# Performance work log

Hardware: AMD Instinct MI355X
Metric: run time of the kernel (lower is better)

The kernel has to match this reference:

```python
import jax, jax.numpy as jnp
import numpy as np

N, D, F, M, K = 4096, 1024, 4096, 2048, 307
EPS = 1e-5

def _ln(h, g, b):
    mu = jnp.mean(h, axis=-1, keepdims=True)
    var = jnp.mean(jnp.square(h - mu), axis=-1, keepdims=True)
    return (h - mu) * jax.lax.rsqrt(var + EPS) * g + b

def _attn(h, wq, wk, wv, mask):
    # wq/wk/wv stored as [D, D] so y = h @ w matches torch Linear(h) with W.T
    q = h @ wq
    k = h @ wk
    v = h @ wv
    s = (q @ k.T) * (1.0 / np.sqrt(D))  # [N, N]
    s = jnp.where(mask, -1e9, s)
    a = jax.nn.softmax(s, axis=-1)
    return a @ v, a

def _ffn(h, w1, b1, w2, b2):
    return jax.nn.gelu(h @ w1 + b1, approximate=False) @ w2 + b2

def setup_inputs() -> dict:
    ks = jax.random.split(jax.random.key(0), 32)
    s = 0.02
    p = lambda i, shape: (jax.random.normal(ks[i], shape, jnp.float32) * s)
    inp = {
        'x': jax.random.normal(ks[0], (N, D), jnp.float32),
        'real_edge_mask': jax.random.bernoulli(ks[1], 0.5, (N, N)),
        'fake_edge_mask': jax.random.bernoulli(ks[2], 0.5, (N, N)),
        'mask_nodes': jax.random.permutation(ks[3], N)[:M].astype(jnp.int32),
        'gene_idx': jnp.argsort(jax.random.uniform(ks[4], (M, D)), axis=-1)[:, :K].astype(jnp.int32),
        'wq1': p(5, (D, D)), 'wk1': p(6, (D, D)), 'wv1': p(7, (D, D)),
        'g1': jnp.ones((D,)), 'be1': jnp.zeros((D,)),
        'fw1': p(8, (D, F)), 'fb1': jnp.zeros((F,)),
        'fw2': p(9, (F, D)), 'fb2': jnp.zeros((D,)),
        'g2': jnp.ones((D,)), 'be2': jnp.zeros((D,)),
        'wq2': p(10, (D, D)), 'wk2': p(11, (D, D)), 'wv2': p(12, (D, D)),
        'g3': jnp.ones((D,)), 'be3': jnp.zeros((D,)),
        'hw1': p(13, (D, F)), 'hb1': jnp.zeros((F,)),
        'hw2': p(14, (F, D)), 'hb2': jnp.zeros((D,)),
        'g4': jnp.ones((D,)), 'be4': jnp.zeros((D,)),
        'head_w': p(15, (D, D)), 'head_b': jnp.zeros((D,)),
    }
    return inp

def reference(x, real_edge_mask, fake_edge_mask, mask_nodes, gene_idx,
              wq1, wk1, wv1, g1, be1, fw1, fb1, fw2, fb2, g2, be2,
              wq2, wk2, wv2, g3, be3, hw1, hb1, hw2, hb2, g4, be4,
              head_w, head_b):
    rows = jnp.arange(M)[:, None]  # [M, 1]
    # encoding_mask_nodes: zero K genes in each of M masked cells
    mask_x = x[mask_nodes].at[rows, gene_idx].set(0.0)
    use_x = x.at[mask_nodes].set(mask_x)

    hidden, encode_weights = _attn(use_x, wq1, wk1, wv1, real_edge_mask)
    hidden = _ln(hidden + use_x, g1, be1)
    hidden = _ln(hidden + _ffn(hidden, fw1, fb1, fw2, fb2), g2, be2)
    # NOTE: original `hidden[mask_nodes][gene_mask] = 0` is a no-op (copy), reproduced.

    recon, _decode_weights = _attn(hidden, wq2, wk2, wv2, real_edge_mask)
    recon = _ln(recon + hidden, g3, be3)
    recon = _ln(recon + _ffn(recon, hw1, hb1, hw2, hb2), g4, be4)
    h = recon @ head_w + head_b

    x_init = x[mask_nodes][rows, gene_idx]   # [M, K]
    x_recon = h[mask_nodes][rows, gene_idx]  # [M, K]
    return x_init, x_recon, encode_weights, recon
```

## Files before the change

kernel.cpp:

```cpp
#include <hip/hip_runtime.h>
#include <math.h>
#include <stdint.h>

typedef unsigned short u16;
typedef __attribute__((ext_vector_type(8))) short bf16x8;
typedef __attribute__((ext_vector_type(4))) float f32x4;
typedef __attribute__((ext_vector_type(4))) unsigned short u16x4;

#define N_ 4096
#define D_ 1024
#define F_ 4096
#define M_ 2048
#define KG 307

__device__ __forceinline__ u16 f2bf(float f) {
  unsigned int u = __float_as_uint(f);
  unsigned int r = u + 0x7fffu + ((u >> 16) & 1u);
  return (u16)(r >> 16);
}

__device__ __forceinline__ float bf2f(u16 u) {
  return __uint_as_float((unsigned)u << 16);
}

__device__ __forceinline__ void gl_lds16(const u16* g, u16* l) {
  __builtin_amdgcn_global_load_lds(
      (__attribute__((address_space(1))) void*)(void*)g,
      (__attribute__((address_space(3))) void*)(void*)l,
      16, 0, 0);
}

enum { E_QKV = 0, E_SMASK = 1, E_PART = 2, E_GELU = 3 };
#define SMEM_BYTES 131072

template <int EPI>
__global__ __launch_bounds__(512, 2) void gemm256(
    const u16* __restrict__ A, const u16* __restrict__ B,
    void* __restrict__ C, void* __restrict__ C2,
    int gridM, int gridN, int Ndim, int Ksp, int lda, int ldb, long zstr,
    const float* __restrict__ bias, const unsigned char* __restrict__ mask,
    float scale) {
  extern __shared__ __align__(16) char smem[];
  const int tid = threadIdx.x;
  const int lane = tid & 63;
  const int wid = tid >> 6;
  const int wr = wid >> 2;
  const int wc = wid & 3;
  const int lr = lane & 15;
  const int lk = lane >> 4;

  const int nwg = gridM * gridN;
  const int bid = blockIdx.x;
  const int q8 = nwg >> 3, r8 = nwg & 7;
  const int xcd = bid & 7, ii = bid >> 3;
  int wg = (xcd < r8 ? xcd * (q8 + 1) : r8 * (q8 + 1) + (xcd - r8) * q8) + ii;
  const int rowblk = wg / (gridN << 2);
  const int rem = wg - rowblk * (gridN << 2);
  const int mrem = gridM - (rowblk << 2);
  int mtile, ntile;
  if (mrem >= 4) {
    ntile = rem >> 2;
    mtile = (rowblk << 2) + (rem & 3);
  } else {
    ntile = rem / mrem;
    mtile = (rowblk << 2) + (rem - ntile * mrem);
  }
  const long bm = (long)mtile * 256;
  const long bn = (long)ntile * 256;
  const long koff = (long)blockIdx.y * Ksp;
  const int NT = Ksp >> 6;

  auto stA = [&](int t, int h) {
    char* base = smem + ((t & 1) << 15) + (h << 14);
    const long k0 = koff + ((long)t << 6);
#pragma unroll
    for (int j = 0; j < 2; ++j) {
      int o = tid + (j << 9);
      int r = o >> 3, s = o & 7;
      gl_lds16(A + (bm + (h << 7) + r) * (long)lda + k0 + ((s ^ (r & 7)) << 3),
               (u16*)(base + o * 16));
    }
  };
  auto stB = [&](int t, int h) {
    char* base = smem + 65536 + ((t & 1) << 15) + (h << 14);
    const long k0 = koff + ((long)t << 6);
#pragma unroll
    for (int j = 0; j < 2; ++j) {
      int o = tid + (j << 9);
      int r = o >> 3, s = o & 7;
      gl_lds16(B + (bn + (h << 7) + r) * (long)ldb + k0 + ((s ^ (r & 7)) << 3),
               (u16*)(base + o * 16));
    }
  };

  bf16x8 avA[2][2], avB[2][2], bv[4][2];
  f32x4 acc[8][4];
#pragma unroll
  for (int m = 0; m < 8; ++m)
#pragma unroll
    for (int n = 0; n < 4; ++n) acc[m][n] = f32x4{0.f, 0.f, 0.f, 0.f};

  auto rdAV = [&](bf16x8(&av)[2][2], const char* Ab_, int q) {
#pragma unroll
    for (int e = 0; e < 2; ++e)
#pragma unroll
      for (int ks = 0; ks < 2; ++ks) {
        int r = (wr << 7) + (q << 5) + (e << 4) + lr;
        av[e][ks] = *(const bf16x8*)(Ab_ + r * 128 + ((((ks << 2) | lk) ^ (r & 7)) << 4));
      }
  };
  auto rdBV = [&](const char* Bb_) {
#pragma unroll
    for (int n = 0; n < 4; ++n)
#pragma unroll
      for (int ks = 0; ks < 2; ++ks) {
        int r = (wc << 6) + (n << 4) + lr;
        bv[n][ks] = *(const bf16x8*)(Bb_ + r * 128 + ((((ks << 2) | lk) ^ (r & 7)) << 4));
      }
  };

#define MM(Q, AV)                                                              \
  __builtin_amdgcn_s_setprio(1);                                               \
  _Pragma("unroll") for (int e = 0; e < 2; ++e)                                \
  _Pragma("unroll") for (int n = 0; n < 4; ++n)                                \
  _Pragma("unroll") for (int ks = 0; ks < 2; ++ks)                             \
      acc[((Q) << 1) | e][n] = __builtin_amdgcn_mfma_f32_16x16x32_bf16(        \
          AV[e][ks], bv[n][ks], acc[((Q) << 1) | e][n], 0, 0, 0);              \
  __builtin_amdgcn_s_setprio(0);                                               \
  __builtin_amdgcn_sched_barrier(0);

  stA(0, 0);
  stA(0, 1);
  stB(0, 0);
  stB(0, 1);
  if (NT > 1) {
    stB(1, 0);
    stB(1, 1);
  }
  __builtin_amdgcn_sched_barrier(0);
  if (NT > 1)
    asm volatile("s_waitcnt vmcnt(4)");
  else
    asm volatile("s_waitcnt vmcnt(0)");
  __builtin_amdgcn_sched_barrier(0);
  __builtin_amdgcn_s_barrier();
  rdAV(avA, smem, 0);
  __builtin_amdgcn_sched_barrier(0);

  for (int t = 0; t < NT; ++t) {
    const char* Ab = smem + ((t & 1) << 15);
    const char* AbN = smem + (((t + 1) & 1) << 15);
    const char* Bb = smem + 65536 + ((t & 1) << 15);
    rdBV(Bb);
    rdAV(avB, Ab, 1);
    if (t + 1 < NT) stA(t + 1, 0);
    __builtin_amdgcn_sched_barrier(0);
    asm volatile("s_waitcnt lgkmcnt(4)");
    __builtin_amdgcn_sched_barrier(0);
    MM(0, avA)
    rdAV(avA, Ab, 2);
    if (t + 1 < NT) stA(t + 1, 1);
    __builtin_amdgcn_sched_barrier(0);
    asm volatile("s_waitcnt lgkmcnt(4)");
    __builtin_amdgcn_sched_barrier(0);
    MM(1, avB)
    __builtin_amdgcn_s_barrier();
    rdAV(avB, Ab, 3);
    if (t + 2 < NT) stB(t + 2, 0);
    __builtin_amdgcn_sched_barrier(0);
    asm volatile("s_waitcnt lgkmcnt(4)");
    __builtin_amdgcn_sched_barrier(0);
    MM(2, avA)
    asm volatile("s_waitcnt lgkmcnt(0)");
    if (t + 2 < NT)
      asm volatile("s_waitcnt vmcnt(2)");
    else
      asm volatile("s_waitcnt vmcnt(0)");
    __builtin_amdgcn_sched_barrier(0);
    __builtin_amdgcn_s_barrier();
    if (t + 1 < NT) rdAV(avA, AbN, 0);
    if (t + 2 < NT) stB(t + 2, 1);
    __builtin_amdgcn_sched_barrier(0);
    MM(3, avB)
  }
#undef MM

  const bool z0 = (blockIdx.y == 0);
#pragma unroll
  for (int m = 0; m < 8; ++m) {
#pragma unroll
    for (int n = 0; n < 4; ++n) {
#pragma unroll
      for (int j = 0; j < 4; ++j) {
        long row = bm + (wr << 7) + (m << 4) + (lk << 2) + j;
        long col = bn + (wc << 6) + (n << 4) + lr;
        float v = acc[m][n][j];
        if constexpr (EPI == E_QKV) {
          if (col < 2048)
            ((u16*)C)[row * 2048 + col] = f2bf(v);
          else
            ((u16*)C2)[(col - 2048) * (long)N_ + row] = f2bf(v);
        } else if constexpr (EPI == E_SMASK) {
          v *= scale;
          if (mask[row * Ndim + col]) v = -1e9f;
          ((u16*)C)[row * Ndim + col] = f2bf(v);
        } else if constexpr (EPI == E_PART) {
          ((u16*)C)[(long)blockIdx.y * zstr + row * Ndim + col] =
              f2bf(v + ((z0 && bias) ? bias[col] : 0.f));
        } else if constexpr (EPI == E_GELU) {
          float tv = v + bias[col];
          float gl = 0.5f * tv * (1.0f + erff(tv * 0.70710678118654752f));
          ((u16*)C)[row * Ndim + col] = f2bf(gl);
        }
      }
    }
  }
}

__global__ __launch_bounds__(256) void gemm_nt_bias(
    const u16* __restrict__ A, const u16* __restrict__ B, float* __restrict__ C,
    int Ndim, int K, int lda, int ldb, const float* __restrict__ bias) {
  __shared__ u16 As[2][128 * 32];
  __shared__ u16 Bs[2][128 * 32];
  const int tid = threadIdx.x;
  const int lane = tid & 63;
  const int wid = tid >> 6;
  const int wr = wid >> 1;
  const int wc = wid & 1;
  const int lr = lane & 15;
  const int lk = lane >> 4;
  const long bm = (long)blockIdx.x * 128;
  const long bn = (long)blockIdx.y * 128;

  f32x4 acc[4][4];
#pragma unroll
  for (int i = 0; i < 4; ++i)
#pragma unroll
    for (int j = 0; j < 4; ++j) acc[i][j] = f32x4{0.f, 0.f, 0.f, 0.f};

  auto stage = [&](int buf, long k0) {
#pragma unroll
    for (int i = 0; i < 2; ++i) {
      int c = tid + i * 256;
      gl_lds16(A + (bm + (c >> 2)) * (long)lda + k0 + (c & 3) * 8, As[buf] + c * 8);
    }
#pragma unroll
    for (int i = 0; i < 2; ++i) {
      int c = tid + i * 256;
      gl_lds16(B + (bn + (c >> 2)) * (long)ldb + k0 + (c & 3) * 8, Bs[buf] + c * 8);
    }
  };

  stage(0, 0);
  __syncthreads();
  const int nt = K / 32;
  int cur = 0;
  for (int t = 0; t < nt; ++t) {
    if (t + 1 < nt) stage(cur ^ 1, (long)(t + 1) * 32);
    bf16x8 av[4], bv[4];
#pragma unroll
    for (int mr = 0; mr < 4; ++mr)
      av[mr] = *(const bf16x8*)(As[cur] + (wr * 64 + mr * 16 + lr) * 32 + lk * 8);
#pragma unroll
    for (int nr = 0; nr < 4; ++nr)
      bv[nr] = *(const bf16x8*)(Bs[cur] + (wc * 64 + nr * 16 + lr) * 32 + lk * 8);
#pragma unroll
    for (int mr = 0; mr < 4; ++mr)
#pragma unroll
      for (int nr = 0; nr < 4; ++nr)
        acc[mr][nr] = __builtin_amdgcn_mfma_f32_16x16x32_bf16(av[mr], bv[nr], acc[mr][nr], 0, 0, 0);
    __syncthreads();
    cur ^= 1;
  }
#pragma unroll
  for (int mr = 0; mr < 4; ++mr)
#pragma unroll
    for (int nr = 0; nr < 4; ++nr)
#pragma unroll
      for (int j = 0; j < 4; ++j) {
        long row = bm + wr * 64 + mr * 16 + lk * 4 + j;
        long col = bn + wc * 64 + nr * 16 + lr;
        C[row * Ndim + col] = acc[mr][nr][j] + bias[col];
      }
}

__global__ __launch_bounds__(256) void tcvt3(const float* __restrict__ in0,
                                             const float* __restrict__ in1,
                                             const float* __restrict__ in2,
                                             u16* __restrict__ out, int R, int C) {
  __shared__ float tile[32][33];
  const float* in = (blockIdx.z == 0) ? in0 : (blockIdx.z == 1 ? in1 : in2);
  u16* dst = out + (size_t)blockIdx.z * R * C;
  int bx = blockIdx.x * 32;
  int by = blockIdx.y * 32;
  int tx = threadIdx.x & 31;
  int ty = threadIdx.x >> 5;
#pragma unroll
  for (int i = 0; i < 32; i += 8)
    tile[ty + i][tx] = in[(long)(by + ty + i) * C + bx + tx];
  __syncthreads();
#pragma unroll
  for (int i = 0; i < 32; i += 8)
    dst[(long)(bx + ty + i) * R + by + tx] = f2bf(tile[tx][ty + i]);
}

__global__ void copy_usex(const float* __restrict__ x, float* __restrict__ xf,
                          u16* __restrict__ xb, long n) {
  long i = (long)blockIdx.x * blockDim.x + threadIdx.x;
  if (i < n) {
    float v = x[i];
    xf[i] = v;
    xb[i] = f2bf(v);
  }
}

__global__ void mask_zero(const float* __restrict__ x, const int* __restrict__ mask_nodes,
                          const int* __restrict__ gene_idx, float* __restrict__ xf,
                          u16* __restrict__ xb, float* __restrict__ x_init) {
  int m = blockIdx.x;
  int k = threadIdx.x;
  if (k >= KG) return;
  int row = mask_nodes[m];
  int col = gene_idx[m * KG + k];
  x_init[m * KG + k] = x[(long)row * D_ + col];
  xf[(long)row * D_ + col] = 0.f;
  xb[(long)row * D_ + col] = 0;
}

template <int NY>
__global__ __launch_bounds__(256) void add_ln(const u16* __restrict__ y, long ystr,
                                              const float* __restrict__ r,
                                              const float* __restrict__ g,
                                              const float* __restrict__ b,
                                              float* __restrict__ of, u16* __restrict__ ob) {
  int row = blockIdx.x;
  const int gi = threadIdx.x * 4;
  const long base = (long)row * D_ + gi;
  f32x4 rv = *(const f32x4*)(r + base);
  u16x4 yv[NY];
#pragma unroll
  for (int z = 0; z < NY; ++z) yv[z] = *(const u16x4*)(y + z * ystr + base);
  float v[4];
  float s = 0.f, ss = 0.f;
#pragma unroll
  for (int i = 0; i < 4; ++i) {
    float t = rv[i];
#pragma unroll
    for (int z = 0; z < NY; ++z) t += bf2f(yv[z][i]);
    v[i] = t;
    s += t;
    ss += t * t;
  }
#pragma unroll
  for (int o = 32; o > 0; o >>= 1) {
    s += __shfl_down(s, o, 64);
    ss += __shfl_down(ss, o, 64);
  }
  __shared__ float red[8];
  int wid = threadIdx.x >> 6, lane = threadIdx.x & 63;
  if (lane == 0) {
    red[wid] = s;
    red[4 + wid] = ss;
  }
  __syncthreads();
  if (threadIdx.x == 0) {
    red[0] = red[0] + red[1] + red[2] + red[3];
    red[4] = red[4] + red[5] + red[6] + red[7];
  }
  __syncthreads();
  float mu = red[0] * (1.f / D_);
  float var = red[4] * (1.f / D_) - mu * mu;
  float rs = rsqrtf(var + 1e-5f);
  f32x4 gv = *(const f32x4*)(g + gi);
  f32x4 bv = *(const f32x4*)(b + gi);
  f32x4 ov;
  u16x4 obv;
#pragma unroll
  for (int i = 0; i < 4; ++i) {
    float o = (v[i] - mu) * rs * gv[i] + bv[i];
    ov[i] = o;
    obv[i] = f2bf(o);
  }
  *(f32x4*)(of + base) = ov;
  *(u16x4*)(ob + base) = obv;
}

template <bool WF32>
__global__ __launch_bounds__(256) void softmax_row(const u16* __restrict__ sin,
                                                   float* __restrict__ a32,
                                                   u16* __restrict__ a16) {
  int row = blockIdx.x;
  const long base = (long)row * N_ + threadIdx.x * 16;
  const u16* sr = sin + base;
  float v[16];
  bf16x8 h0 = *(const bf16x8*)(sr);
  bf16x8 h1 = *(const bf16x8*)(sr + 8);
#pragma unroll
  for (int j = 0; j < 8; ++j) {
    v[j] = bf2f((u16)h0[j]);
    v[8 + j] = bf2f((u16)h1[j]);
  }
  float mx = v[0];
#pragma unroll
  for (int i = 1; i < 16; ++i) mx = fmaxf(mx, v[i]);
#pragma unroll
  for (int o = 32; o > 0; o >>= 1) mx = fmaxf(mx, __shfl_down(mx, o, 64));
  __shared__ float red[8];
  int wid = threadIdx.x >> 6, lane = threadIdx.x & 63;
  if (lane == 0) red[wid] = mx;
  __syncthreads();
  if (threadIdx.x == 0) red[0] = fmaxf(fmaxf(red[0], red[1]), fmaxf(red[2], red[3]));
  __syncthreads();
  mx = red[0];
  float sum = 0.f;
#pragma unroll
  for (int i = 0; i < 16; ++i) {
    v[i] = __expf(v[i] - mx);
    sum += v[i];
  }
#pragma unroll
  for (int o = 32; o > 0; o >>= 1) sum += __shfl_down(sum, o, 64);
  if (lane == 0) red[4 + wid] = sum;
  __syncthreads();
  if (threadIdx.x == 0) red[4] = red[4] + red[5] + red[6] + red[7];
  __syncthreads();
  float inv = 1.f / red[4];
  bf16x8 o0, o1;
#pragma unroll
  for (int j = 0; j < 8; ++j) {
    float p0 = v[j] * inv, p1 = v[8 + j] * inv;
    o0[j] = (short)f2bf(p0);
    o1[j] = (short)f2bf(p1);
    if constexpr (WF32) {
      a32[base + j] = p0;
      a32[base + 8 + j] = p1;
    }
  }
  *(bf16x8*)(a16 + base) = o0;
  *(bf16x8*)(a16 + base + 8) = o1;
}

__global__ void gather_rows(const u16* __restrict__ src, const int* __restrict__ mask_nodes,
                            u16* __restrict__ dst) {
  int m = blockIdx.x;
  int row = mask_nodes[m];
  for (int i = threadIdx.x; i < D_; i += 256)
    dst[(long)m * D_ + i] = src[(long)row * D_ + i];
}

__global__ void gather_recon(const float* __restrict__ h, const int* __restrict__ gene_idx,
                             float* __restrict__ xr) {
  int m = blockIdx.x;
  int k = threadIdx.x;
  if (k >= KG) return;
  xr[m * KG + k] = h[(long)m * D_ + gene_idx[m * KG + k]];
}

extern "C" void kernel_launch(void* const* d_in, const int* in_sizes, int n_in,
                              void* d_out, int out_size, void* d_ws, size_t ws_size,
                              hipStream_t stream) {
  const float* x = (const float*)d_in[0];
  const unsigned char* real_mask = (const unsigned char*)d_in[1];
  const int* mask_nodes = (const int*)d_in[3];
  const int* gene_idx = (const int*)d_in[4];
  const float* wq1 = (const float*)d_in[5];
  const float* wk1 = (const float*)d_in[6];
  const float* wv1 = (const float*)d_in[7];
  const float* g1 = (const float*)d_in[8];
  const float* be1 = (const float*)d_in[9];
  const float* fw1 = (const float*)d_in[10];
  const float* fb1 = (const float*)d_in[11];
  const float* fw2 = (const float*)d_in[12];
  const float* fb2 = (const float*)d_in[13];
  const float* g2 = (const float*)d_in[14];
  const float* be2 = (const float*)d_in[15];
  const float* wq2 = (const float*)d_in[16];
  const float* wk2 = (const float*)d_in[17];
  const float* wv2 = (const float*)d_in[18];
  const float* g3 = (const float*)d_in[19];
  const float* be3 = (const float*)d_in[20];
  const float* hw1 = (const float*)d_in[21];
  const float* hb1 = (const float*)d_in[22];
  const float* hw2 = (const float*)d_in[23];
  const float* hb2 = (const float*)d_in[24];
  const float* g4 = (const float*)d_in[25];
  const float* be4 = (const float*)d_in[26];
  const float* head_w = (const float*)d_in[27];
  const float* head_b = (const float*)d_in[28];

  float* out_xinit = (float*)d_out;
  float* out_xrecon = out_xinit + (long)M_ * KG;
  float* out_enc = out_xrecon + (long)M_ * KG;
  float* out_recon = out_enc + (long)N_ * N_;

  hipFuncSetAttribute((const void*)gemm256<E_QKV>, hipFuncAttributeMaxDynamicSharedMemorySize, SMEM_BYTES);
  hipFuncSetAttribute((const void*)gemm256<E_SMASK>, hipFuncAttributeMaxDynamicSharedMemorySize, SMEM_BYTES);
  hipFuncSetAttribute((const void*)gemm256<E_PART>, hipFuncAttributeMaxDynamicSharedMemorySize, SMEM_BYTES);
  hipFuncSetAttribute((const void*)gemm256<E_GELU>, hipFuncAttributeMaxDynamicSharedMemorySize, SMEM_BYTES);

  char* w = (char*)d_ws;
  size_t off = 0;
  auto alloc = [&](size_t bytes) {
    void* p = w + off;
    off += (bytes + 255) & ~(size_t)255;
    return p;
  };
  float* useXf = (float*)alloc((size_t)N_ * D_ * 4);
  u16* useXb = (u16*)alloc((size_t)N_ * D_ * 2);
  u16* wslot = (u16*)alloc((size_t)D_ * F_ * 2);
  u16* qkb = (u16*)alloc((size_t)N_ * 2048 * 2);
  u16* vT = (u16*)alloc((size_t)D_ * N_ * 2);
  u16* tbuf = (u16*)alloc((size_t)N_ * F_ * 2);
  u16* aB = (u16*)alloc((size_t)N_ * N_ * 2);
  u16* gout4b = (u16*)alloc((size_t)4 * N_ * D_ * 2);
  float* actA = (float*)alloc((size_t)N_ * D_ * 4);
  float* actB = (float*)alloc((size_t)N_ * D_ * 4);
  u16* actB16 = (u16*)alloc((size_t)N_ * D_ * 2);
  u16* AgB = qkb;

  const float scale = 1.0f / 32.0f;
  const long nd = (long)N_ * D_;
  dim3 blk(256), blk5(512);

  copy_usex<<<dim3((unsigned)((nd + 255) / 256)), blk, 0, stream>>>(x, useXf, useXb, nd);
  mask_zero<<<dim3(M_), 320, 0, stream>>>(x, mask_nodes, gene_idx, useXf, useXb, out_xinit);

#define TCVT1(src, R, C, dst) \
  tcvt3<<<dim3((C) / 32, (R) / 32, 1), blk, 0, stream>>>(src, src, src, dst, R, C)
#define TCVTQ(s0, s1, s2, dst) \
  tcvt3<<<dim3(32, 32, 3), blk, 0, stream>>>(s0, s1, s2, dst, 1024, 1024)
#define G256(EP, GM, GN, Z, A, B, C, C2, ND, KS, LA, LB, ZS, BI, MK, SC)                        \
  gemm256<EP><<<dim3((GM) * (GN), Z), blk5, SMEM_BYTES, stream>>>(A, B, C, C2, GM, GN, ND, KS, \
                                                                  LA, LB, ZS, BI, MK, SC)

  TCVTQ(wq1, wk1, wv1, wslot);
  G256(E_QKV, 16, 12, 1, useXb, wslot, qkb, vT, 3072, 1024, 1024, 1024, 0, nullptr, nullptr, 0.f);
  G256(E_SMASK, 16, 16, 1, qkb, qkb + 1024, aB, nullptr, 4096, 1024, 2048, 2048, 0, nullptr, real_mask, scale);
  softmax_row<true><<<dim3(N_), blk, 0, stream>>>(aB, out_enc, aB);
  G256(E_PART, 16, 4, 4, aB, vT, gout4b, nullptr, 1024, 1024, 4096, 4096, nd, nullptr, nullptr, 0.f);
  add_ln<4><<<dim3(N_), blk, 0, stream>>>(gout4b, nd, useXf, g1, be1, actA, actB16);
  TCVT1(fw1, D_, F_, wslot);
  G256(E_GELU, 16, 16, 1, actB16, wslot, tbuf, nullptr, 4096, 1024, 1024, 1024, 0, fb1, nullptr, 0.f);
  TCVT1(fw2, F_, D_, wslot);
  G256(E_PART, 16, 4, 4, tbuf, wslot, gout4b, nullptr, 1024, 1024, 4096, 4096, nd, fb2, nullptr, 0.f);
  add_ln<4><<<dim3(N_), blk, 0, stream>>>(gout4b, nd, actA, g2, be2, actB, actB16);

  TCVTQ(wq2, wk2, wv2, wslot);
  G256(E_QKV, 16, 12, 1, actB16, wslot, qkb, vT, 3072, 1024, 1024, 1024, 0, nullptr, nullptr, 0.f);
  G256(E_SMASK, 16, 16, 1, qkb, qkb + 1024, aB, nullptr, 4096, 1024, 2048, 2048, 0, nullptr, real_mask, scale);
  softmax_row<false><<<dim3(N_), blk, 0, stream>>>(aB, nullptr, aB);
  G256(E_PART, 16, 4, 4, aB, vT, gout4b, nullptr, 1024, 1024, 4096, 4096, nd, nullptr, nullptr, 0.f);
  add_ln<4><<<dim3(N_), blk, 0, stream>>>(gout4b, nd, actB, g3, be3, actA, actB16);
  TCVT1(hw1, D_, F_, wslot);
  G256(E_GELU, 16, 16, 1, actB16, wslot, tbuf, nullptr, 4096, 1024, 1024, 1024, 0, hb1, nullptr, 0.f);
  TCVT1(hw2, F_, D_, wslot);
  G256(E_PART, 16, 4, 4, tbuf, wslot, gout4b, nullptr, 1024, 1024, 4096, 4096, nd, hb2, nullptr, 0.f);
  add_ln<4><<<dim3(N_), blk, 0, stream>>>(gout4b, nd, actA, g4, be4, out_recon, actB16);

  gather_rows<<<dim3(M_), blk, 0, stream>>>(actB16, mask_nodes, AgB);
  TCVT1(head_w, D_, D_, wslot);
  gemm_nt_bias<<<dim3(16, 8), blk, 0, stream>>>(AgB, wslot, actA, 1024, 1024, 1024, 1024, head_b);
  gather_recon<<<dim3(M_), 320, 0, stream>>>(actA, gene_idx, out_xrecon);
#undef TCVT1
#undef TCVTQ
#undef G256
}
```

Baseline: 660.6 us.

## Use 256x192 tiles for QKV GEMM and polynomial erf for GELU epilogue

The GEMM kernel is templated on the N tile width. The QKV projection now runs with 256x192 tiles, giving 256 workgroups instead of 192 so the grid fills the GPU more evenly. B tile staging is split into 64-row chunks, and the prefetch schedule and waitcnt values are updated to match. Separately, the GELU epilogue replaces erff with an Abramowitz-Stegun polynomial using rcp and exp, which is cheaper but slightly less accurate.

```diff
diff --git a/kernel.cpp b/kernel.cpp
--- a/kernel.cpp
+++ b/kernel.cpp
@@ -23,6 +23,19 @@
   return __uint_as_float((unsigned)u << 16);
 }
 
+__device__ __forceinline__ float gelu_fast(float t) {
+  float x = t * 0.70710678118654752f;
+  float ax = fabsf(x);
+  float u = __builtin_amdgcn_rcpf(fmaf(0.3275911f, ax, 1.0f));
+  float poly =
+      u * fmaf(u, fmaf(u, fmaf(u, fmaf(u, 1.061405429f, -1.453152027f), 1.421413741f),
+                       -0.284496736f),
+               0.254829592f);
+  float erfabs = fmaf(-poly, __expf(-ax * ax), 1.0f);
+  float er = copysignf(erfabs, x);
+  return 0.5f * t * (1.0f + er);
+}
+
 __device__ __forceinline__ void gl_lds16(const u16* g, u16* l) {
   __builtin_amdgcn_global_load_lds(
       (__attribute__((address_space(1))) void*)(void*)g,
@@ -33,13 +46,17 @@
 enum { E_QKV = 0, E_SMASK = 1, E_PART = 2, E_GELU = 3 };
 #define SMEM_BYTES 131072
 
-template <int EPI>
+template <int EPI, int TN = 256>
 __global__ __launch_bounds__(512, 2) void gemm256(
     const u16* __restrict__ A, const u16* __restrict__ B,
     void* __restrict__ C, void* __restrict__ C2,
     int gridM, int gridN, int Ndim, int Ksp, int lda, int ldb, long zstr,
     const float* __restrict__ bias, const unsigned char* __restrict__ mask,
     float scale) {
+  constexpr int NV = TN / 64;
+  constexpr int WCOLS = TN / 4;
+  constexpr int NBCH = TN / 64;
+  constexpr int BBYTES = TN * 128;
   extern __shared__ __align__(16) char smem[];
   const int tid = threadIdx.x;
   const int lane = tid & 63;
@@ -66,7 +83,7 @@
     mtile = (rowblk << 2) + (rem - ntile * mrem);
   }
   const long bm = (long)mtile * 256;
-  const long bn = (long)ntile * 256;
+  const long bn = (long)ntile * TN;
   const long koff = (long)blockIdx.y * Ksp;
   const int NT = Ksp >> 6;
 
@@ -81,24 +98,21 @@
                (u16*)(base + o * 16));
     }
   };
-  auto stB = [&](int t, int h) {
-    char* base = smem + 65536 + ((t & 1) << 15) + (h << 14);
+  auto stB = [&](int t, int c) {
+    char* base = smem + 65536 + (t & 1) * BBYTES + (c << 13);
     const long k0 = koff + ((long)t << 6);
-#pragma unroll
-    for (int j = 0; j < 2; ++j) {
-      int o = tid + (j << 9);
-      int r = o >> 3, s = o & 7;
-      gl_lds16(B + (bn + (h << 7) + r) * (long)ldb + k0 + ((s ^ (r & 7)) << 3),
-               (u16*)(base + o * 16));
-    }
+    int o = tid;
+    int r = o >> 3, s = o & 7;
+    gl_lds16(B + (bn + (c << 6) + r) * (long)ldb + k0 + ((s ^ (r & 7)) << 3),
+             (u16*)(base + o * 16));
   };
 
-  bf16x8 avA[2][2], avB[2][2], bv[4][2];
-  f32x4 acc[8][4];
+  bf16x8 avA[2][2], avB[2][2], bv[NV][2];
+  f32x4 acc[8][NV];
 #pragma unroll
   for (int m = 0; m < 8; ++m)
 #pragma unroll
-    for (int n = 0; n < 4; ++n) acc[m][n] = f32x4{0.f, 0.f, 0.f, 0.f};
+    for (int n = 0; n < NV; ++n) acc[m][n] = f32x4{0.f, 0.f, 0.f, 0.f};
 
   auto rdAV = [&](bf16x8(&av)[2][2], const char* Ab_, int q) {
 #pragma unroll
@@ -111,10 +125,10 @@
   };
   auto rdBV = [&](const char* Bb_) {
 #pragma unroll
-    for (int n = 0; n < 4; ++n)
+    for (int n = 0; n < NV; ++n)
 #pragma unroll
       for (int ks = 0; ks < 2; ++ks) {
-        int r = (wc << 6) + (n << 4) + lr;
+        int r = wc * WCOLS + (n << 4) + lr;
         bv[n][ks] = *(const bf16x8*)(Bb_ + r * 128 + ((((ks << 2) | lk) ^ (r & 7)) << 4));
       }
   };
@@ -122,7 +136,7 @@
 #define MM(Q, AV)                                                              \
   __builtin_amdgcn_s_setprio(1);                                               \
   _Pragma("unroll") for (int e = 0; e < 2; ++e)                                \
-  _Pragma("unroll") for (int n = 0; n < 4; ++n)                                \
+  _Pragma("unroll") for (int n = 0; n < NV; ++n)                               \
   _Pragma("unroll") for (int ks = 0; ks < 2; ++ks)                             \
       acc[((Q) << 1) | e][n] = __builtin_amdgcn_mfma_f32_16x16x32_bf16(        \
           AV[e][ks], bv[n][ks], acc[((Q) << 1) | e][n], 0, 0, 0);              \
@@ -131,17 +145,17 @@
 
   stA(0, 0);
   stA(0, 1);
-  stB(0, 0);
-  stB(0, 1);
+#pragma unroll
+  for (int c = 0; c < NBCH; ++c) stB(0, c);
   if (NT > 1) {
-    stB(1, 0);
-    stB(1, 1);
-  }
-  __builtin_amdgcn_sched_barrier(0);
-  if (NT > 1)
-    asm volatile("s_waitcnt vmcnt(4)");
-  else
+#pragma unroll
+    for (int c = 0; c < NBCH; ++c) stB(1, c);
+    __builtin_amdgcn_sched_barrier(0);
+    asm volatile("s_waitcnt vmcnt(%0)" ::"i"(NBCH));
+  } else {
+    __builtin_amdgcn_sched_barrier(0);
     asm volatile("s_waitcnt vmcnt(0)");
+  }
   __builtin_amdgcn_sched_barrier(0);
   __builtin_amdgcn_s_barrier();
   rdAV(avA, smem, 0);
@@ -150,7 +164,7 @@
   for (int t = 0; t < NT; ++t) {
     const char* Ab = smem + ((t & 1) << 15);
     const char* AbN = smem + (((t + 1) & 1) << 15);
-    const char* Bb = smem + 65536 + ((t & 1) << 15);
+    const char* Bb = smem + 65536 + (t & 1) * BBYTES;
     rdBV(Bb);
     rdAV(avB, Ab, 1);
     if (t + 1 < NT) stA(t + 1, 0);
@@ -166,7 +180,10 @@
     MM(1, avB)
     __builtin_amdgcn_s_barrier();
     rdAV(avB, Ab, 3);
-    if (t + 2 < NT) stB(t + 2, 0);
+    if (t + 2 < NT) {
+      stB(t + 2, 0);
+      stB(t + 2, 1);
+    }
     __builtin_amdgcn_sched_barrier(0);
     asm volatile("s_waitcnt lgkmcnt(4)");
     __builtin_amdgcn_sched_barrier(0);
@@ -179,7 +196,10 @@
     __builtin_amdgcn_sched_barrier(0);
     __builtin_amdgcn_s_barrier();
     if (t + 1 < NT) rdAV(avA, AbN, 0);
-    if (t + 2 < NT) stB(t + 2, 1);
+    if (t + 2 < NT) {
+#pragma unroll
+      for (int c = 2; c < NBCH; ++c) stB(t + 2, c);
+    }
     __builtin_amdgcn_sched_barrier(0);
     MM(3, avB)
   }
@@ -189,11 +209,11 @@
 #pragma unroll
   for (int m = 0; m < 8; ++m) {
 #pragma unroll
-    for (int n = 0; n < 4; ++n) {
+    for (int n = 0; n < NV; ++n) {
 #pragma unroll
       for (int j = 0; j < 4; ++j) {
         long row = bm + (wr << 7) + (m << 4) + (lk << 2) + j;
-        long col = bn + (wc << 6) + (n << 4) + lr;
+        long col = bn + wc * WCOLS + (n << 4) + lr;
         float v = acc[m][n][j];
         if constexpr (EPI == E_QKV) {
           if (col < 2048)
@@ -208,9 +228,7 @@
           ((u16*)C)[(long)blockIdx.y * zstr + row * Ndim + col] =
               f2bf(v + ((z0 && bias) ? bias[col] : 0.f));
         } else if constexpr (EPI == E_GELU) {
-          float tv = v + bias[col];
-          float gl = 0.5f * tv * (1.0f + erff(tv * 0.70710678118654752f));
-          ((u16*)C)[row * Ndim + col] = f2bf(gl);
+          ((u16*)C)[row * Ndim + col] = f2bf(gelu_fast(v + bias[col]));
         }
       }
     }
@@ -493,7 +511,7 @@
   float* out_enc = out_xrecon + (long)M_ * KG;
   float* out_recon = out_enc + (long)N_ * N_;
 
-  hipFuncSetAttribute((const void*)gemm256<E_QKV>, hipFuncAttributeMaxDynamicSharedMemorySize, SMEM_BYTES);
+  hipFuncSetAttribute((const void*)gemm256<E_QKV, 192>, hipFuncAttributeMaxDynamicSharedMemorySize, SMEM_BYTES);
   hipFuncSetAttribute((const void*)gemm256<E_SMASK>, hipFuncAttributeMaxDynamicSharedMemorySize, SMEM_BYTES);
   hipFuncSetAttribute((const void*)gemm256<E_PART>, hipFuncAttributeMaxDynamicSharedMemorySize, SMEM_BYTES);
   hipFuncSetAttribute((const void*)gemm256<E_GELU>, hipFuncAttributeMaxDynamicSharedMemorySize, SMEM_BYTES);
@@ -529,12 +547,15 @@
   tcvt3<<<dim3((C) / 32, (R) / 32, 1), blk, 0, stream>>>(src, src, src, dst, R, C)
 #define TCVTQ(s0, s1, s2, dst) \
   tcvt3<<<dim3(32, 32, 3), blk, 0, stream>>>(s0, s1, s2, dst, 1024, 1024)
+#define GQKV(A)                                                                           \
+  gemm256<E_QKV, 192><<<dim3(256, 1), blk5, SMEM_BYTES, stream>>>(                        \
+      A, wslot, qkb, vT, 16, 16, 3072, 1024, 1024, 1024, 0, nullptr, nullptr, 0.f)
 #define G256(EP, GM, GN, Z, A, B, C, C2, ND, KS, LA, LB, ZS, BI, MK, SC)                        \
   gemm256<EP><<<dim3((GM) * (GN), Z), blk5, SMEM_BYTES, stream>>>(A, B, C, C2, GM, GN, ND, KS, \
                                                                   LA, LB, ZS, BI, MK, SC)
 
   TCVTQ(wq1, wk1, wv1, wslot);
-  G256(E_QKV, 16, 12, 1, useXb, wslot, qkb, vT, 3072, 1024, 1024, 1024, 0, nullptr, nullptr, 0.f);
+  GQKV(useXb);
   G256(E_SMASK, 16, 16, 1, qkb, qkb + 1024, aB, nullptr, 4096, 1024, 2048, 2048, 0, nullptr, real_mask, scale);
   softmax_row<true><<<dim3(N_), blk, 0, stream>>>(aB, out_enc, aB);
   G256(E_PART, 16, 4, 4, aB, vT, gout4b, nullptr, 1024, 1024, 4096, 4096, nd, nullptr, nullptr, 0.f);
@@ -546,7 +567,7 @@
   add_ln<4><<<dim3(N_), blk, 0, stream>>>(gout4b, nd, actA, g2, be2, actB, actB16);
 
   TCVTQ(wq2, wk2, wv2, wslot);
-  G256(E_QKV, 16, 12, 1, actB16, wslot, qkb, vT, 3072, 1024, 1024, 1024, 0, nullptr, nullptr, 0.f);
+  GQKV(actB16);
   G256(E_SMASK, 16, 16, 1, qkb, qkb + 1024, aB, nullptr, 4096, 1024, 2048, 2048, 0, nullptr, real_mask, scale);
   softmax_row<false><<<dim3(N_), blk, 0, stream>>>(aB, nullptr, aB);
   G256(E_PART, 16, 4, 4, aB, vT, gout4b, nullptr, 1024, 1024, 4096, 4096, nd, nullptr, nullptr, 0.f);
@@ -563,5 +584,6 @@
   gather_recon<<<dim3(M_), 320, 0, stream>>>(actA, gene_idx, out_xrecon);
 #undef TCVT1
 #undef TCVTQ
+#undef GQKV
 #undef G256
 }
```

Measured after the change: 623.5 us. -5.6%, faster.
